# Kernel tuning notes

Hardware: AMD Instinct MI355X
Metric: run time of the kernel (lower is better)

Reference implementation:

```python
import jax, jax.numpy as jnp
import numpy as np

N_HEAD = 16
MASK_NEG = -10000.0


def setup_inputs() -> dict:
    key = jax.random.key(0)
    k1, k2, k3 = jax.random.split(key, 3)
    B, S, D = 4, 2048, 1024
    x = jax.random.normal(k1, (B, S, D), dtype=jnp.float32)
    c_attn_w = jax.random.normal(k2, (D, 3 * D), dtype=jnp.float32) * 0.02
    c_attn_b = jnp.zeros((3 * D,), dtype=jnp.float32)
    c_proj_w = jax.random.normal(k3, (D, D), dtype=jnp.float32) * 0.02
    c_proj_b = jnp.zeros((D,), dtype=jnp.float32)
    return {"x": x, "c_attn_w": c_attn_w, "c_attn_b": c_attn_b,
            "c_proj_w": c_proj_w, "c_proj_b": c_proj_b}


def reference(x, c_attn_w, c_attn_b, c_proj_w, c_proj_b):
    B, S, D = x.shape
    H = N_HEAD
    Dh = D // H
    # fused QKV projection (Conv1D = x @ W + b)
    qkv = x @ c_attn_w + c_attn_b          # [B,S,3D]
    q, k, v = jnp.split(qkv, 3, axis=-1)   # each [B,S,D]
    # split heads -> [B,H,S,Dh]
    q = q.reshape(B, S, H, Dh).transpose(0, 2, 1, 3)
    k = k.reshape(B, S, H, Dh).transpose(0, 2, 1, 3)
    v = v.reshape(B, S, H, Dh).transpose(0, 2, 1, 3)
    # scores with scaling (scale=True)
    w = jnp.einsum('bhqd,bhkd->bhqk', q, k) / jnp.sqrt(jnp.float32(Dh))
    # multiplicative causal mask: w*b + -10000*(1-b)
    b = jnp.tril(jnp.ones((S, S), dtype=w.dtype))[None, None]  # [1,1,S,S]
    w = w * b + MASK_NEG * (1.0 - b)
    w = jax.nn.softmax(w, axis=-1)
    # dropout is identity at inference
    a = jnp.einsum('bhqk,bhkd->bhqd', w, v)  # [B,H,S,Dh]
    a = a.transpose(0, 2, 1, 3).reshape(B, S, D)  # merge heads
    out = a @ c_proj_w + c_proj_b
    return out
```

## Files before the change

kernel.cpp:

```cpp
#include <hip/hip_runtime.h>

typedef unsigned short u16;
typedef short bf16x8 __attribute__((ext_vector_type(8)));
typedef float f32x4 __attribute__((ext_vector_type(4)));
typedef unsigned int u32;
typedef u32 u32x4 __attribute__((ext_vector_type(4)));

#define B_ 4
#define S_ 2048
#define D_ 1024
#define H_ 16
#define DH_ 64
#define M_ 8192
#define SCL2E 0.1803368801111244f

__device__ __forceinline__ u16 f2b(float f) {
  union { float f; unsigned int u; } v; v.f = f;
  unsigned int u = v.u;
  unsigned int r = (u + 0x7FFFu + ((u >> 16) & 1u)) >> 16;
  return (u16)r;
}

__device__ __forceinline__ void gload16(const void* g, void* l) {
  __builtin_amdgcn_global_load_lds(
      (const __attribute__((address_space(1))) unsigned int*)g,
      (__attribute__((address_space(3))) unsigned int*)l,
      16, 0, 0);
}

__device__ __forceinline__ u32 cvt_pk_bf16(float lo, float hi) {
  u32 r;
  asm("v_cvt_pk_bf16_f32 %0, %1, %2" : "=v"(r) : "v"(lo), "v"(hi));
  return r;
}

struct __attribute__((aligned(8))) u16x4 { u16 x, y, z, w; };

__global__ void cvt_f32_bf16(const float* __restrict__ in, u16* __restrict__ out, int n) {
  int i = (blockIdx.x * blockDim.x + threadIdx.x) * 4;
  if (i >= n) return;
  float4 v = *(const float4*)(in + i);
  u16x4 o; o.x = f2b(v.x); o.y = f2b(v.y); o.z = f2b(v.z); o.w = f2b(v.w);
  *(u16x4*)(out + i) = o;
}

__global__ void transpose_cvt(const float* __restrict__ in, u16* __restrict__ out, int R, int C) {
  __shared__ float tile[32][33];
  int c0 = blockIdx.x * 32, r0 = blockIdx.y * 32;
  int tx = threadIdx.x, ty = threadIdx.y;
#pragma unroll
  for (int j = 0; j < 32; j += 8)
    tile[ty + j][tx] = in[(size_t)(r0 + ty + j) * C + c0 + tx];
  __syncthreads();
#pragma unroll
  for (int j = 0; j < 32; j += 8)
    out[(size_t)(c0 + ty + j) * R + r0 + tx] = f2b(tile[tx][ty + j]);
}

template <int MODE>
__global__ __launch_bounds__(256) void gemm_bt(
    const u16* __restrict__ A, const u16* __restrict__ BT,
    const float* __restrict__ bias, float* __restrict__ outf,
    u16* __restrict__ qb, u16* __restrict__ kb, u16* __restrict__ vtb,
    int Ncols, int Kdim) {
  __shared__ __attribute__((aligned(16))) u16 lsA[2][128 * 64];
  __shared__ __attribute__((aligned(16))) u16 lsB[2][128 * 64];
  const int t = threadIdx.x;
  const int lane = t & 63, w = t >> 6;
  const int lhi = lane >> 4, llo = lane & 15;

  const int gx = gridDim.x;
  const int lin = blockIdx.y * gx + blockIdx.x;
  const int nwg = gx * gridDim.y;
  const int sw = (lin & 7) * (nwg >> 3) + (lin >> 3);
  const int m0 = (sw / gx) * 128, n0 = (sw % gx) * 128;

  const int wr = (w >> 1) * 64, wc = (w & 1) * 64;

  const int r8 = lane >> 3;
  const int scolE = ((lane & 7) ^ r8) * 8;
  const int srow = w * 32 + r8;

  f32x4 acc[4][4] = {};
  const int nt = Kdim >> 6;

#define STAGE_G(buf, kk0)                                                        \
  _Pragma("unroll") for (int j = 0; j < 4; ++j) {                                \
    gload16(A + (size_t)(m0 + srow + j * 8) * Kdim + (kk0) + scolE,              \
            &lsA[buf][(w * 32 + j * 8) * 64]);                                   \
    gload16(BT + (size_t)(n0 + srow + j * 8) * Kdim + (kk0) + scolE,             \
            &lsB[buf][(w * 32 + j * 8) * 64]);                                   \
  }

  STAGE_G(0, 0)

  for (int tt = 0; tt < nt; ++tt) {
    const int cur = tt & 1;
    if (tt + 1 < nt) {
      STAGE_G(cur ^ 1, (tt + 1) << 6)
      asm volatile("s_waitcnt vmcnt(8)" ::: "memory");
    } else {
      asm volatile("s_waitcnt vmcnt(0)" ::: "memory");
    }
    __builtin_amdgcn_sched_barrier(0);
    __builtin_amdgcn_s_barrier();
    __builtin_amdgcn_sched_barrier(0);
#pragma unroll
    for (int kk = 0; kk < 2; ++kk) {
      bf16x8 af[4], bfr[4];
#pragma unroll
      for (int i = 0; i < 4; ++i) {
        int ra = wr + i * 16 + llo;
        af[i] = *(const bf16x8*)((const char*)&lsA[cur][ra * 64] +
                                 ((kk * 64 + lhi * 16) ^ ((ra & 7) << 4)));
        int rb = wc + i * 16 + llo;
        bfr[i] = *(const bf16x8*)((const char*)&lsB[cur][rb * 64] +
                                  ((kk * 64 + lhi * 16) ^ ((rb & 7) << 4)));
      }
#pragma unroll
      for (int mi = 0; mi < 4; ++mi)
#pragma unroll
        for (int ni = 0; ni < 4; ++ni)
          acc[mi][ni] = __builtin_amdgcn_mfma_f32_16x16x32_bf16(af[mi], bfr[ni], acc[mi][ni], 0, 0, 0);
    }
    __builtin_amdgcn_sched_barrier(0);
    __builtin_amdgcn_s_barrier();
  }
#undef STAGE_G

  if (MODE == 0) {
#pragma unroll
    for (int mi = 0; mi < 4; ++mi)
#pragma unroll
      for (int ni = 0; ni < 4; ++ni)
#pragma unroll
        for (int r = 0; r < 4; ++r) {
          int m = m0 + wr + mi * 16 + lhi * 4 + r;
          int n = n0 + wc + ni * 16 + llo;
          outf[(size_t)m * Ncols + n] = acc[mi][ni][r] + bias[n];
        }
  } else if (n0 < 1024) {
#pragma unroll
    for (int mi = 0; mi < 4; ++mi)
#pragma unroll
      for (int ni = 0; ni < 4; ++ni)
#pragma unroll
        for (int r = 0; r < 4; ++r) {
          int m = m0 + wr + mi * 16 + lhi * 4 + r;
          int n = n0 + wc + ni * 16 + llo;
          int bidx = m >> 11, s = m & 2047, hh = n >> 6, dh = n & 63;
          qb[((size_t)(bidx * 16 + hh) * 2048 + s) * 64 + dh] =
              f2b((acc[mi][ni][r] + bias[n]) * SCL2E);
        }
  } else if (n0 < 2048) {
#pragma unroll
    for (int mi = 0; mi < 4; ++mi)
#pragma unroll
      for (int ni = 0; ni < 4; ++ni)
#pragma unroll
        for (int r = 0; r < 4; ++r) {
          int m = m0 + wr + mi * 16 + lhi * 4 + r;
          int n2 = n0 - 1024 + wc + ni * 16 + llo;
          int bidx = m >> 11, s = m & 2047, hh = n2 >> 6, dh = n2 & 63;
          kb[((size_t)(bidx * 16 + hh) * 2048 + s) * 64 + dh] =
              f2b(acc[mi][ni][r] + bias[n0 + wc + ni * 16 + llo]);
        }
  } else {
#pragma unroll
    for (int mi = 0; mi < 4; ++mi)
#pragma unroll
      for (int ni = 0; ni < 4; ++ni)
#pragma unroll
        for (int r = 0; r < 4; ++r) {
          int m = m0 + wr + mi * 16 + lhi * 4 + r;
          int n2 = n0 - 2048 + wc + ni * 16 + llo;
          int bidx = m >> 11, s = m & 2047, hh = n2 >> 6, dh = n2 & 63;
          int col = (s & ~127) | ((s & 15) * 8 + ((s >> 4) & 7));
          vtb[((size_t)(bidx * 16 + hh) * 64 + dh) * 2048 + col] =
              f2b(acc[mi][ni][r] + bias[n0 + wc + ni * 16 + llo]);
        }
  }
}

__global__ __launch_bounds__(512) void attn128(
    const u16* __restrict__ Qb, const u16* __restrict__ Kb,
    const u16* __restrict__ VTb, u16* __restrict__ AO) {
  __shared__ __attribute__((aligned(16))) u16 kls[128 * 64];
  __shared__ __attribute__((aligned(16))) u16 vls[64 * 128];
  __shared__ __attribute__((aligned(16))) u16 pl[8][16][136];
  const int t = threadIdx.x, w = t >> 6, lane = t & 63;
  const int lhi = lane >> 4, llo = lane & 15;
  const int bh = blockIdx.y, bb = bh >> 4, hh = bh & 15;
  const u16* Qp = Qb + (size_t)bh * (S_ * DH_);
  const u16* Kp = Kb + (size_t)bh * (S_ * DH_);
  const u16* Vp = VTb + (size_t)bh * (DH_ * S_);
  const int pr = blockIdx.x;

  bf16x8 ones;
#pragma unroll
  for (int i = 0; i < 8; ++i) ones[i] = (short)0x3F80;

  int krow[2], kcolE[2], kdst[2], vrow[2], vcolE[2], vdst[2];
#pragma unroll
  for (int c = 0; c < 2; ++c) {
    int b = c * 8192 + t * 16;
    krow[c] = b >> 7;
    kcolE[c] = (b & 127) >> 1;
    kdst[c] = krow[c] * 128 + ((b & 127) ^ ((krow[c] & 7) << 4));
    vrow[c] = b >> 8;
    vcolE[c] = (b & 255) >> 1;
    vdst[c] = vrow[c] * 256 + ((b & 255) ^ ((vrow[c] & 15) << 4));
  }

  for (int ci = 0; ci < 2; ++ci) {
    const int qc = ci ? (15 - pr) : pr;
    const int q0 = qc * 128;
    const int qrow = q0 + w * 16 + llo;
    bf16x8 aq0 = *(const bf16x8*)(Qp + (size_t)qrow * DH_ + lhi * 8);
    bf16x8 aq1 = *(const bf16x8*)(Qp + (size_t)qrow * DH_ + 32 + lhi * 8);
    const int n128 = qc + 1;

    bf16x8 kst[2], vst[2];
#pragma unroll
    for (int c = 0; c < 2; ++c) {
      kst[c] = *(const bf16x8*)(Kp + (size_t)krow[c] * DH_ + kcolE[c]);
      vst[c] = *(const bf16x8*)(Vp + (size_t)vrow[c] * S_ + vcolE[c]);
    }
    __syncthreads();
#pragma unroll
    for (int c = 0; c < 2; ++c) {
      *(bf16x8*)((char*)kls + kdst[c]) = kst[c];
      *(bf16x8*)((char*)vls + vdst[c]) = vst[c];
    }
    __syncthreads();

    f32x4 o[4] = {};
    f32x4 osum = {};
    const int crow = q0 + w * 16 + lhi * 4;

    for (int tt = 0; tt < n128; ++tt) {
      const int kv0 = tt << 7;
      const bool pf = (tt + 1 < n128);

      f32x4 sc[8] = {};
      const int sw = (llo & 7) << 4;
      __builtin_amdgcn_s_setprio(1);
#pragma unroll
      for (int f = 0; f < 8; ++f) {
        const char* base = (const char*)kls + (f * 16 + llo) * 128;
        bf16x8 bk0 = *(const bf16x8*)(base + ((lhi * 16) ^ sw));
        bf16x8 bk1 = *(const bf16x8*)(base + ((64 + lhi * 16) ^ sw));
        sc[f] = __builtin_amdgcn_mfma_f32_16x16x32_bf16(aq0, bk0, sc[f], 0, 0, 0);
        sc[f] = __builtin_amdgcn_mfma_f32_16x16x32_bf16(aq1, bk1, sc[f], 0, 0, 0);
      }
      __builtin_amdgcn_s_setprio(0);

      if (pf) {
#pragma unroll
        for (int c = 0; c < 2; ++c) {
          kst[c] = *(const bf16x8*)(Kp + (size_t)(kv0 + 128 + krow[c]) * DH_ + kcolE[c]);
          vst[c] = *(const bf16x8*)(Vp + (size_t)vrow[c] * S_ + kv0 + 128 + vcolE[c]);
        }
      }

      const bool lastit = (tt == n128 - 1);
#pragma unroll
      for (int r = 0; r < 4; ++r) {
        float p[8];
#pragma unroll
        for (int f = 0; f < 8; ++f) {
          float x = sc[f][r];
          if (lastit && (kv0 + f * 16 + llo > crow + r)) x = -1e30f;
          p[f] = exp2f(x);
        }
        u32x4 pw;
        pw[0] = cvt_pk_bf16(p[0], p[1]);
        pw[1] = cvt_pk_bf16(p[2], p[3]);
        pw[2] = cvt_pk_bf16(p[4], p[5]);
        pw[3] = cvt_pk_bf16(p[6], p[7]);
        *(u32x4*)((char*)&pl[w][lhi * 4 + r][0] + llo * 16) = pw;
      }

      __builtin_amdgcn_s_setprio(1);
#pragma unroll
      for (int kk = 0; kk < 4; ++kk) {
        bf16x8 ap = *(const bf16x8*)((const char*)&pl[w][llo][0] + kk * 64 + lhi * 16);
#pragma unroll
        for (int f = 0; f < 4; ++f) {
          const char* vbase = (const char*)vls + (f * 16 + llo) * 256;
          bf16x8 bv = *(const bf16x8*)(vbase + ((kk * 64 + lhi * 16) ^ (llo << 4)));
          o[f] = __builtin_amdgcn_mfma_f32_16x16x32_bf16(ap, bv, o[f], 0, 0, 0);
        }
        osum = __builtin_amdgcn_mfma_f32_16x16x32_bf16(ap, ones, osum, 0, 0, 0);
      }
      __builtin_amdgcn_s_setprio(0);

      if (pf) {
        __syncthreads();
#pragma unroll
        for (int c = 0; c < 2; ++c) {
          *(bf16x8*)((char*)kls + kdst[c]) = kst[c];
          *(bf16x8*)((char*)vls + vdst[c]) = vst[c];
        }
        __syncthreads();
      }
    }

#pragma unroll
    for (int f = 0; f < 4; ++f)
#pragma unroll
      for (int r = 0; r < 4; ++r) {
        int row = crow + r;
        int dh = f * 16 + llo;
        float val = o[f][r] / osum[r];
        AO[((size_t)bb * S_ + row) * D_ + hh * DH_ + dh] = f2b(val);
      }
  }
}

extern "C" void kernel_launch(void* const* d_in, const int* in_sizes, int n_in,
                              void* d_out, int out_size, void* d_ws, size_t ws_size,
                              hipStream_t stream) {
  const float* x  = (const float*)d_in[0];
  const float* w1 = (const float*)d_in[1];
  const float* b1 = (const float*)d_in[2];
  const float* w2 = (const float*)d_in[3];
  const float* b2 = (const float*)d_in[4];
  float* out = (float*)d_out;
  char* ws = (char*)d_ws;

  u16* xb  = (u16*)(ws);
  u16* w1t = (u16*)(ws + 16777216);
  u16* w2t = (u16*)(ws + 23068672);
  u16* qb  = (u16*)(ws + 25165824);
  u16* kb  = (u16*)(ws + 41943040);
  u16* vtb = (u16*)(ws + 58720256);
  u16* ao  = xb;

  cvt_f32_bf16<<<8192, 256, 0, stream>>>(x, xb, M_ * D_);
  transpose_cvt<<<dim3(96, 32), dim3(32, 8), 0, stream>>>(w1, w1t, 1024, 3072);
  transpose_cvt<<<dim3(32, 32), dim3(32, 8), 0, stream>>>(w2, w2t, 1024, 1024);

  gemm_bt<1><<<dim3(24, 64), 256, 0, stream>>>(xb, w1t, b1, nullptr, qb, kb, vtb, 3072, 1024);
  attn128<<<dim3(8, 64), 512, 0, stream>>>(qb, kb, vtb, ao);
  gemm_bt<0><<<dim3(8, 64), 256, 0, stream>>>(ao, w2t, b2, out, nullptr, nullptr, nullptr, 1024, 1024);
}
```

Before: 189.1 us.

## Use 8 waves per GEMM tile and peel last causal attention iteration

```diff
diff --git a/kernel.cpp b/kernel.cpp
--- a/kernel.cpp
+++ b/kernel.cpp
@@ -58,7 +58,7 @@
 }
 
 template <int MODE>
-__global__ __launch_bounds__(256) void gemm_bt(
+__global__ __launch_bounds__(512) void gemm_bt(
     const u16* __restrict__ A, const u16* __restrict__ BT,
     const float* __restrict__ bias, float* __restrict__ outf,
     u16* __restrict__ qb, u16* __restrict__ kb, u16* __restrict__ vtb,
@@ -75,21 +75,20 @@
   const int sw = (lin & 7) * (nwg >> 3) + (lin >> 3);
   const int m0 = (sw / gx) * 128, n0 = (sw % gx) * 128;
 
-  const int wr = (w >> 1) * 64, wc = (w & 1) * 64;
+  const int wr = (w >> 2) * 64, wc = (w & 3) * 32;
 
   const int r8 = lane >> 3;
   const int scolE = ((lane & 7) ^ r8) * 8;
-  const int srow = w * 32 + r8;
-
-  f32x4 acc[4][4] = {};
+
+  f32x4 acc[4][2] = {};
   const int nt = Kdim >> 6;
 
 #define STAGE_G(buf, kk0)                                                        \
-  _Pragma("unroll") for (int j = 0; j < 4; ++j) {                                \
-    gload16(A + (size_t)(m0 + srow + j * 8) * Kdim + (kk0) + scolE,              \
-            &lsA[buf][(w * 32 + j * 8) * 64]);                                   \
-    gload16(BT + (size_t)(n0 + srow + j * 8) * Kdim + (kk0) + scolE,             \
-            &lsB[buf][(w * 32 + j * 8) * 64]);                                   \
+  _Pragma("unroll") for (int j = 0; j < 2; ++j) {                                \
+    gload16(A + (size_t)(m0 + j * 64 + w * 8 + r8) * Kdim + (kk0) + scolE,       \
+            &lsA[buf][j * 4096 + w * 512]);                                      \
+    gload16(BT + (size_t)(n0 + j * 64 + w * 8 + r8) * Kdim + (kk0) + scolE,      \
+            &lsB[buf][j * 4096 + w * 512]);                                      \
   }
 
   STAGE_G(0, 0)
@@ -98,7 +97,7 @@
     const int cur = tt & 1;
     if (tt + 1 < nt) {
       STAGE_G(cur ^ 1, (tt + 1) << 6)
-      asm volatile("s_waitcnt vmcnt(8)" ::: "memory");
+      asm volatile("s_waitcnt vmcnt(4)" ::: "memory");
     } else {
       asm volatile("s_waitcnt vmcnt(0)" ::: "memory");
     }
@@ -107,21 +106,26 @@
     __builtin_amdgcn_sched_barrier(0);
 #pragma unroll
     for (int kk = 0; kk < 2; ++kk) {
-      bf16x8 af[4], bfr[4];
+      bf16x8 af[4], bfr[2];
 #pragma unroll
       for (int i = 0; i < 4; ++i) {
         int ra = wr + i * 16 + llo;
         af[i] = *(const bf16x8*)((const char*)&lsA[cur][ra * 64] +
                                  ((kk * 64 + lhi * 16) ^ ((ra & 7) << 4)));
-        int rb = wc + i * 16 + llo;
-        bfr[i] = *(const bf16x8*)((const char*)&lsB[cur][rb * 64] +
+      }
+#pragma unroll
+      for (int p = 0; p < 2; ++p) {
+        int rb = wc + p * 16 + llo;
+        bfr[p] = *(const bf16x8*)((const char*)&lsB[cur][rb * 64] +
                                   ((kk * 64 + lhi * 16) ^ ((rb & 7) << 4)));
       }
+      __builtin_amdgcn_s_setprio(1);
 #pragma unroll
       for (int mi = 0; mi < 4; ++mi)
 #pragma unroll
-        for (int ni = 0; ni < 4; ++ni)
+        for (int ni = 0; ni < 2; ++ni)
           acc[mi][ni] = __builtin_amdgcn_mfma_f32_16x16x32_bf16(af[mi], bfr[ni], acc[mi][ni], 0, 0, 0);
+      __builtin_amdgcn_s_setprio(0);
     }
     __builtin_amdgcn_sched_barrier(0);
     __builtin_amdgcn_s_barrier();
@@ -132,7 +136,7 @@
 #pragma unroll
     for (int mi = 0; mi < 4; ++mi)
 #pragma unroll
-      for (int ni = 0; ni < 4; ++ni)
+      for (int ni = 0; ni < 2; ++ni)
 #pragma unroll
         for (int r = 0; r < 4; ++r) {
           int m = m0 + wr + mi * 16 + lhi * 4 + r;
@@ -143,7 +147,7 @@
 #pragma unroll
     for (int mi = 0; mi < 4; ++mi)
 #pragma unroll
-      for (int ni = 0; ni < 4; ++ni)
+      for (int ni = 0; ni < 2; ++ni)
 #pragma unroll
         for (int r = 0; r < 4; ++r) {
           int m = m0 + wr + mi * 16 + lhi * 4 + r;
@@ -156,28 +160,30 @@
 #pragma unroll
     for (int mi = 0; mi < 4; ++mi)
 #pragma unroll
-      for (int ni = 0; ni < 4; ++ni)
+      for (int ni = 0; ni < 2; ++ni)
 #pragma unroll
         for (int r = 0; r < 4; ++r) {
           int m = m0 + wr + mi * 16 + lhi * 4 + r;
-          int n2 = n0 - 1024 + wc + ni * 16 + llo;
+          int n = n0 + wc + ni * 16 + llo;
+          int n2 = n - 1024;
           int bidx = m >> 11, s = m & 2047, hh = n2 >> 6, dh = n2 & 63;
           kb[((size_t)(bidx * 16 + hh) * 2048 + s) * 64 + dh] =
-              f2b(acc[mi][ni][r] + bias[n0 + wc + ni * 16 + llo]);
+              f2b(acc[mi][ni][r] + bias[n]);
         }
   } else {
 #pragma unroll
     for (int mi = 0; mi < 4; ++mi)
 #pragma unroll
-      for (int ni = 0; ni < 4; ++ni)
+      for (int ni = 0; ni < 2; ++ni)
 #pragma unroll
         for (int r = 0; r < 4; ++r) {
           int m = m0 + wr + mi * 16 + lhi * 4 + r;
-          int n2 = n0 - 2048 + wc + ni * 16 + llo;
+          int n = n0 + wc + ni * 16 + llo;
+          int n2 = n - 2048;
           int bidx = m >> 11, s = m & 2047, hh = n2 >> 6, dh = n2 & 63;
           int col = (s & ~127) | ((s & 15) * 8 + ((s >> 4) & 7));
           vtb[((size_t)(bidx * 16 + hh) * 64 + dh) * 2048 + col] =
-              f2b(acc[mi][ni][r] + bias[n0 + wc + ni * 16 + llo]);
+              f2b(acc[mi][ni][r] + bias[n]);
         }
   }
 }
@@ -237,13 +243,18 @@
     f32x4 o[4] = {};
     f32x4 osum = {};
     const int crow = q0 + w * 16 + lhi * 4;
-
-    for (int tt = 0; tt < n128; ++tt) {
+    const int sw = (llo & 7) << 4;
+
+    for (int tt = 0; tt < n128 - 1; ++tt) {
       const int kv0 = tt << 7;
-      const bool pf = (tt + 1 < n128);
+
+#pragma unroll
+      for (int c = 0; c < 2; ++c) {
+        kst[c] = *(const bf16x8*)(Kp + (size_t)(kv0 + 128 + krow[c]) * DH_ + kcolE[c]);
+        vst[c] = *(const bf16x8*)(Vp + (size_t)vrow[c] * S_ + kv0 + 128 + vcolE[c]);
+      }
 
       f32x4 sc[8] = {};
-      const int sw = (llo & 7) << 4;
       __builtin_amdgcn_s_setprio(1);
 #pragma unroll
       for (int f = 0; f < 8; ++f) {
@@ -255,24 +266,11 @@
       }
       __builtin_amdgcn_s_setprio(0);
 
-      if (pf) {
-#pragma unroll
-        for (int c = 0; c < 2; ++c) {
-          kst[c] = *(const bf16x8*)(Kp + (size_t)(kv0 + 128 + krow[c]) * DH_ + kcolE[c]);
-          vst[c] = *(const bf16x8*)(Vp + (size_t)vrow[c] * S_ + kv0 + 128 + vcolE[c]);
-        }
-      }
-
-      const bool lastit = (tt == n128 - 1);
 #pragma unroll
       for (int r = 0; r < 4; ++r) {
         float p[8];
 #pragma unroll
-        for (int f = 0; f < 8; ++f) {
-          float x = sc[f][r];
-          if (lastit && (kv0 + f * 16 + llo > crow + r)) x = -1e30f;
-          p[f] = exp2f(x);
-        }
+        for (int f = 0; f < 8; ++f) p[f] = exp2f(sc[f][r]);
         u32x4 pw;
         pw[0] = cvt_pk_bf16(p[0], p[1]);
         pw[1] = cvt_pk_bf16(p[2], p[3]);
@@ -295,15 +293,59 @@
       }
       __builtin_amdgcn_s_setprio(0);
 
-      if (pf) {
-        __syncthreads();
-#pragma unroll
-        for (int c = 0; c < 2; ++c) {
-          *(bf16x8*)((char*)kls + kdst[c]) = kst[c];
-          *(bf16x8*)((char*)vls + vdst[c]) = vst[c];
-        }
-        __syncthreads();
-      }
+      __syncthreads();
+#pragma unroll
+      for (int c = 0; c < 2; ++c) {
+        *(bf16x8*)((char*)kls + kdst[c]) = kst[c];
+        *(bf16x8*)((char*)vls + vdst[c]) = vst[c];
+      }
+      __syncthreads();
+    }
+
+    {
+      const int kv0 = (n128 - 1) << 7;
+      f32x4 sc[8] = {};
+      __builtin_amdgcn_s_setprio(1);
+#pragma unroll
+      for (int f = 0; f < 8; ++f) {
+        const char* base = (const char*)kls + (f * 16 + llo) * 128;
+        bf16x8 bk0 = *(const bf16x8*)(base + ((lhi * 16) ^ sw));
+        bf16x8 bk1 = *(const bf16x8*)(base + ((64 + lhi * 16) ^ sw));
+        sc[f] = __builtin_amdgcn_mfma_f32_16x16x32_bf16(aq0, bk0, sc[f], 0, 0, 0);
+        sc[f] = __builtin_amdgcn_mfma_f32_16x16x32_bf16(aq1, bk1, sc[f], 0, 0, 0);
+      }
+      __builtin_amdgcn_s_setprio(0);
+
+#pragma unroll
+      for (int r = 0; r < 4; ++r) {
+        float p[8];
+#pragma unroll
+        for (int f = 0; f < 8; ++f) {
+          float x = sc[f][r];
+          if (kv0 + f * 16 + llo > crow + r) x = -1e30f;
+          p[f] = exp2f(x);
+        }
+        u32x4 pw;
+        pw[0] = cvt_pk_bf16(p[0], p[1]);
+        pw[1] = cvt_pk_bf16(p[2], p[3]);
+        pw[2] = cvt_pk_bf16(p[4], p[5]);
+        pw[3] = cvt_pk_bf16(p[6], p[7]);
+        *(u32x4*)((char*)&pl[w][lhi * 4 + r][0] + llo * 16) = pw;
+      }
+
+      __builtin_amdgcn_s_setprio(1);
+#pragma unroll
+      for (int kk = 0; kk < 4; ++kk) {
+        bf16x8 ap = *(const bf16x8*)((const char*)&pl[w][llo][0] + kk * 64 + lhi * 16);
+#pragma unroll
+        for (int f = 0; f < 4; ++f) {
+          const char* vbase = (const char*)vls + (f * 16 + llo) * 256;
+          bf16x8 bv = *(const bf16x8*)(vbase + ((kk * 64 + lhi * 16) ^ (llo << 4)));
+          o[f] = __builtin_amdgcn_mfma_f32_16x16x32_bf16(ap, bv, o[f], 0, 0, 0);
+        }
+        osum = __builtin_amdgcn_mfma_f32_16x16x32_bf16(ap, ones, osum, 0, 0, 0);
+      }
+      __builtin_amdgcn_s_setprio(0);
     }
 
 #pragma unroll
@@ -341,7 +383,7 @@
   transpose_cvt<<<dim3(96, 32), dim3(32, 8), 0, stream>>>(w1, w1t, 1024, 3072);
   transpose_cvt<<<dim3(32, 32), dim3(32, 8), 0, stream>>>(w2, w2t, 1024, 1024);
 
-  gemm_bt<1><<<dim3(24, 64), 256, 0, stream>>>(xb, w1t, b1, nullptr, qb, kb, vtb, 3072, 1024);
+  gemm_bt<1><<<dim3(24, 64), 512, 0, stream>>>(xb, w1t, b1, nullptr, qb, kb, vtb, 3072, 1024);
   attn128<<<dim3(8, 64), 512, 0, stream>>>(qb, kb, vtb, ao);
-  gemm_bt<0><<<dim3(8, 64), 256, 0, stream>>>(ao, w2t, b2, out, nullptr, nullptr, nullptr, 1024, 1024);
-}
+  gemm_bt<0><<<dim3(8, 64), 512, 0, stream>>>(ao, w2t, b2, out, nullptr, nullptr, nullptr, 1024, 1024);
+}
```

After: 212.9 us. 12.6% more time.

## Peel masked last KV tile, issue prefetch early, remap blocks to heads

Applied to the files above, without the earlier changes.

```diff
diff --git a/kernel.cpp b/kernel.cpp
--- a/kernel.cpp
+++ b/kernel.cpp
@@ -190,11 +190,15 @@
   __shared__ __attribute__((aligned(16))) u16 pl[8][16][136];
   const int t = threadIdx.x, w = t >> 6, lane = t & 63;
   const int lhi = lane >> 4, llo = lane & 15;
-  const int bh = blockIdx.y, bb = bh >> 4, hh = bh & 15;
+
+  const int lin = blockIdx.y * 8 + blockIdx.x;
+  const int bh = ((lin >> 6) << 3) | (lin & 7);
+  const int pr = (lin >> 3) & 7;
+  const int bb = bh >> 4, hh = bh & 15;
+
   const u16* Qp = Qb + (size_t)bh * (S_ * DH_);
   const u16* Kp = Kb + (size_t)bh * (S_ * DH_);
   const u16* Vp = VTb + (size_t)bh * (DH_ * S_);
-  const int pr = blockIdx.x;
 
   bf16x8 ones;
 #pragma unroll
@@ -237,13 +241,18 @@
     f32x4 o[4] = {};
     f32x4 osum = {};
     const int crow = q0 + w * 16 + lhi * 4;
-
-    for (int tt = 0; tt < n128; ++tt) {
+    const int sw = (llo & 7) << 4;
+
+    for (int tt = 0; tt < n128 - 1; ++tt) {
       const int kv0 = tt << 7;
-      const bool pf = (tt + 1 < n128);
+
+#pragma unroll
+      for (int c = 0; c < 2; ++c) {
+        kst[c] = *(const bf16x8*)(Kp + (size_t)(kv0 + 128 + krow[c]) * DH_ + kcolE[c]);
+        vst[c] = *(const bf16x8*)(Vp + (size_t)vrow[c] * S_ + kv0 + 128 + vcolE[c]);
+      }
 
       f32x4 sc[8] = {};
-      const int sw = (llo & 7) << 4;
       __builtin_amdgcn_s_setprio(1);
 #pragma unroll
       for (int f = 0; f < 8; ++f) {
@@ -255,24 +264,11 @@
       }
       __builtin_amdgcn_s_setprio(0);
 
-      if (pf) {
-#pragma unroll
-        for (int c = 0; c < 2; ++c) {
-          kst[c] = *(const bf16x8*)(Kp + (size_t)(kv0 + 128 + krow[c]) * DH_ + kcolE[c]);
-          vst[c] = *(const bf16x8*)(Vp + (size_t)vrow[c] * S_ + kv0 + 128 + vcolE[c]);
-        }
-      }
-
-      const bool lastit = (tt == n128 - 1);
 #pragma unroll
       for (int r = 0; r < 4; ++r) {
         float p[8];
 #pragma unroll
-        for (int f = 0; f < 8; ++f) {
-          float x = sc[f][r];
-          if (lastit && (kv0 + f * 16 + llo > crow + r)) x = -1e30f;
-          p[f] = exp2f(x);
-        }
+        for (int f = 0; f < 8; ++f) p[f] = exp2f(sc[f][r]);
         u32x4 pw;
         pw[0] = cvt_pk_bf16(p[0], p[1]);
         pw[1] = cvt_pk_bf16(p[2], p[3]);
@@ -295,15 +291,59 @@
       }
       __builtin_amdgcn_s_setprio(0);
 
-      if (pf) {
-        __syncthreads();
-#pragma unroll
-        for (int c = 0; c < 2; ++c) {
-          *(bf16x8*)((char*)kls + kdst[c]) = kst[c];
-          *(bf16x8*)((char*)vls + vdst[c]) = vst[c];
-        }
-        __syncthreads();
-      }
+      __syncthreads();
+#pragma unroll
+      for (int c = 0; c < 2; ++c) {
+        *(bf16x8*)((char*)kls + kdst[c]) = kst[c];
+        *(bf16x8*)((char*)vls + vdst[c]) = vst[c];
+      }
+      __syncthreads();
+    }
+
+    {
+      const int kv0 = (n128 - 1) << 7;
+      f32x4 sc[8] = {};
+      __builtin_amdgcn_s_setprio(1);
+#pragma unroll
+      for (int f = 0; f < 8; ++f) {
+        const char* base = (const char*)kls + (f * 16 + llo) * 128;
+        bf16x8 bk0 = *(const bf16x8*)(base + ((lhi * 16) ^ sw));
+        bf16x8 bk1 = *(const bf16x8*)(base + ((64 + lhi * 16) ^ sw));
+        sc[f] = __builtin_amdgcn_mfma_f32_16x16x32_bf16(aq0, bk0, sc[f], 0, 0, 0);
+        sc[f] = __builtin_amdgcn_mfma_f32_16x16x32_bf16(aq1, bk1, sc[f], 0, 0, 0);
+      }
+      __builtin_amdgcn_s_setprio(0);
+
+#pragma unroll
+      for (int r = 0; r < 4; ++r) {
+        float p[8];
+#pragma unroll
+        for (int f = 0; f < 8; ++f) {
+          float x = sc[f][r];
+          if (kv0 + f * 16 + llo > crow + r) x = -1e30f;
+          p[f] = exp2f(x);
+        }
+        u32x4 pw;
+        pw[0] = cvt_pk_bf16(p[0], p[1]);
+        pw[1] = cvt_pk_bf16(p[2], p[3]);
+        pw[2] = cvt_pk_bf16(p[4], p[5]);
+        pw[3] = cvt_pk_bf16(p[6], p[7]);
+        *(u32x4*)((char*)&pl[w][lhi * 4 + r][0] + llo * 16) = pw;
+      }
+
+      __builtin_amdgcn_s_setprio(1);
+#pragma unroll
+      for (int kk = 0; kk < 4; ++kk) {
+        bf16x8 ap = *(const bf16x8*)((const char*)&pl[w][llo][0] + kk * 64 + lhi * 16);
+#pragma unroll
+        for (int f = 0; f < 4; ++f) {
+          const char* vbase = (const char*)vls + (f * 16 + llo) * 256;
+          bf16x8 bv = *(const bf16x8*)(vbase + ((kk * 64 + lhi * 16) ^ (llo << 4)));
+          o[f] = __builtin_amdgcn_mfma_f32_16x16x32_bf16(ap, bv, o[f], 0, 0, 0);
+        }
+        osum = __builtin_amdgcn_mfma_f32_16x16x32_bf16(ap, ones, osum, 0, 0, 0);
+      }
+      __builtin_amdgcn_s_setprio(0);
     }
 
 #pragma unroll
```

Measured after the change: 185.5 us. About the same (-1.9%).
